# Kernel tuning notes

Hardware: AMD Instinct MI355X
Metric: run time of the kernel (lower is better)

## Reference

```python
import jax, jax.numpy as jnp
import numpy as np

D_MODEL = 192; D_INNER = 384; N_STATE = 16; D_CONV = 4; DT_RANK = 12; DEPTH = 24
PATCH = 16; STRIDE = 16; IMG = 128; EPS = 1e-5


def _ln(x, w, b):
    m = jnp.mean(x, -1, keepdims=True)
    v = jnp.mean((x - m) ** 2, -1, keepdims=True)
    return (x - m) * jax.lax.rsqrt(v + EPS) * w + b


def _mamba_dir(xz, cw, cb, xpw, dpw, dpb, Alog, Dv):
    # xz: (B, L, 2*d_inner); one direction of the bidirectional Mamba mixer
    xp, z = jnp.split(xz, 2, axis=-1)               # (B,L,di) each
    xc = jnp.transpose(xp, (0, 2, 1))               # (B,di,L)
    xc = jnp.pad(xc, ((0, 0), (0, 0), (D_CONV - 1, 0)))  # causal pad
    xc = jax.lax.conv_general_dilated(
        xc, cw, (1,), 'VALID',
        dimension_numbers=('NCH', 'OIH', 'NCH'),
        feature_group_count=D_INNER) + cb[None, :, None]
    u = jax.nn.silu(jnp.transpose(xc, (0, 2, 1)))   # (B,L,di)
    dbl = u @ xpw.T                                  # (B,L,dt_rank+2N)
    dt, Bm, Cm = jnp.split(dbl, [DT_RANK, DT_RANK + N_STATE], axis=-1)
    dt = jax.nn.softplus(dt @ dpw.T + dpb)           # (B,L,di)
    A = -jnp.exp(Alog)                               # (di,N)
    dA = jnp.exp(dt[..., None] * A)                  # (B,L,di,N)
    dBu = (dt * u)[..., None] * Bm[:, :, None, :]    # (B,L,di,N)

    def comb(c1, c2):
        a1, b1 = c1
        a2, b2 = c2
        return a1 * a2, a2 * b1 + b2

    _, h = jax.lax.associative_scan(comb, (dA, dBu), axis=1)
    y = jnp.einsum('bldn,bln->bld', h, Cm) + u * Dv
    return y * jax.nn.silu(z)


def _forward(x, patch_w, patch_b, ln_w, ln_b, in_w,
             cf_w, cf_b, xpf_w, dtf_w, dtf_b, Alog_f, D_f,
             cbk_w, cbk_b, xpb_w, dtb_w, dtb_b, Alog_b, D_b,
             out_w, nf_w, nf_b, head_w, head_b):
    B = x.shape[0]
    p = jax.lax.conv_general_dilated(
        x, patch_w, (STRIDE,) * 3, 'VALID',
        dimension_numbers=('NCDHW', 'OIDHW', 'NCDHW')) + patch_b[None, :, None, None, None]
    hidden = p.reshape(B, D_MODEL, -1).transpose(0, 2, 1)  # (B, L=512, D)
    residual = jnp.zeros_like(hidden)

    xs = (ln_w, ln_b, in_w, cf_w, cf_b, xpf_w, dtf_w, dtf_b, Alog_f, D_f,
          cbk_w, cbk_b, xpb_w, dtb_w, dtb_b, Alog_b, D_b, out_w)

    def step(carry, pl):
        hidden, residual = carry
        (lw, lb, iw, cfw, cfb, xpf, dwf, dbf, Af, Dfv,
         cbw, cbb, xpb, dwb, dbb, Ab, Dbv, ow) = pl
        residual = residual + hidden
        hn = _ln(residual, lw, lb)
        xz = hn @ iw.T                               # (B,L,2di)
        yf = _mamba_dir(xz, cfw, cfb, xpf, dwf, dbf, Af, Dfv)
        yb = jnp.flip(_mamba_dir(jnp.flip(xz, 1), cbw, cbb, xpb, dwb, dbb, Ab, Dbv), 1)
        hidden = (yf + yb) @ ow.T
        return (hidden, residual), None

    (hidden, residual), _ = jax.lax.scan(step, (hidden, residual), xs)
    final = _ln(residual + hidden, nf_w, nf_b)
    feat = final[:, -1, :]                           # final_pool_type='none' -> last token
    return feat @ head_w.T + head_b


def setup_inputs() -> dict:
    key = jax.random.key(0)
    ks = jax.random.split(key, 16)
    rn = lambda k, s, sc=0.02: jax.random.normal(k, s, jnp.float32) * sc
    d = {}
    d['x'] = jax.random.normal(ks[0], (1, 1, IMG, IMG, IMG), jnp.float32)
    d['patch_w'] = rn(ks[1], (D_MODEL, 1, PATCH, PATCH, PATCH), 0.05)
    d['patch_b'] = jnp.zeros((D_MODEL,), jnp.float32)
    d['ln_w'] = jnp.ones((DEPTH, D_MODEL), jnp.float32)
    d['ln_b'] = jnp.zeros((DEPTH, D_MODEL), jnp.float32)
    d['in_w'] = rn(ks[2], (DEPTH, 2 * D_INNER, D_MODEL))
    d['cf_w'] = rn(ks[3], (DEPTH, D_INNER, 1, D_CONV), 0.2)
    d['cf_b'] = jnp.zeros((DEPTH, D_INNER), jnp.float32)
    d['xpf_w'] = rn(ks[4], (DEPTH, DT_RANK + 2 * N_STATE, D_INNER))
    d['dtf_w'] = rn(ks[5], (DEPTH, D_INNER, DT_RANK), 0.1)
    d['dtf_b'] = jnp.full((DEPTH, D_INNER), -4.6, jnp.float32)  # softplus -> dt~0.01
    d['Alog_f'] = jnp.log(jnp.broadcast_to(jnp.arange(1, N_STATE + 1, dtype=jnp.float32), (DEPTH, D_INNER, N_STATE)))
    d['D_f'] = jnp.ones((DEPTH, D_INNER), jnp.float32)
    d['cbk_w'] = rn(ks[6], (DEPTH, D_INNER, 1, D_CONV), 0.2)
    d['cbk_b'] = jnp.zeros((DEPTH, D_INNER), jnp.float32)
    d['xpb_w'] = rn(ks[7], (DEPTH, DT_RANK + 2 * N_STATE, D_INNER))
    d['dtb_w'] = rn(ks[8], (DEPTH, D_INNER, DT_RANK), 0.1)
    d['dtb_b'] = jnp.full((DEPTH, D_INNER), -4.6, jnp.float32)
    d['Alog_b'] = jnp.log(jnp.broadcast_to(jnp.arange(1, N_STATE + 1, dtype=jnp.float32), (DEPTH, D_INNER, N_STATE)))
    d['D_b'] = jnp.ones((DEPTH, D_INNER), jnp.float32)
    d['out_w'] = rn(ks[9], (DEPTH, D_MODEL, D_INNER))
    d['nf_w'] = jnp.ones((D_MODEL,), jnp.float32)
    d['nf_b'] = jnp.zeros((D_MODEL,), jnp.float32)
    d['head_w'] = rn(ks[10], (2, D_MODEL))
    d['head_b'] = jnp.zeros((2,), jnp.float32)
    return d


def reference(x, patch_w, patch_b, ln_w, ln_b, in_w,
              cf_w, cf_b, xpf_w, dtf_w, dtf_b, Alog_f, D_f,
              cbk_w, cbk_b, xpb_w, dtb_w, dtb_b, Alog_b, D_b,
              out_w, nf_w, nf_b, head_w, head_b):
    return _forward(x, patch_w, patch_b, ln_w, ln_b, in_w,
                    cf_w, cf_b, xpf_w, dtf_w, dtf_b, Alog_f, D_f,
                    cbk_w, cbk_b, xpb_w, dtb_w, dtb_b, Alog_b, D_b,
                    out_w, nf_w, nf_b, head_w, head_b)
```

## Files before the change

kernel.cpp:

```cpp
#include <hip/hip_runtime.h>
#include <hip/hip_bf16.h>

#define D_MODEL 192
#define D_INNER 384
#define N_STATE 16
#define DT_RANK 12
#define DEPTH 24
#define SEQ 512
#define NCHUNK 8
#define CLEN 64
#define TS 68
#define AS 33
#define PART_STRIDE (SEQ * D_MODEL)
#define USTR (SEQ * D_INNER)
#define KSPLIT 16

typedef __hip_bfloat16 bf16;
typedef unsigned short u16;

__device__ __forceinline__ float silu_f(float x) { return x / (1.f + __expf(-x)); }
__device__ __forceinline__ float softplus_f(float x) {
    return (x > 20.f) ? x : log1pf(__expf(x));
}
__device__ __forceinline__ float bf2f(unsigned u) {
    return __uint_as_float(u << 16);
}
__device__ __forceinline__ u16 f2bu(float f) {
    bf16 b = __float2bfloat16(f);
    return *reinterpret_cast<u16*>(&b);
}

template<typename T> __device__ __forceinline__ float ld(const void* p, long i) {
    return ((const float*)p)[i];
}
template<> __device__ __forceinline__ float ld<bf16>(const void* p, long i) {
    return bf2f(((const u16*)p)[i]);
}
template<typename T> __device__ __forceinline__ float4 ld4(const void* p, long i) {
    return *(const float4*)((const float*)p + i);
}
template<> __device__ __forceinline__ float4 ld4<bf16>(const void* p, long i) {
    const ushort4 v = *(const ushort4*)((const u16*)p + i);
    return make_float4(bf2f(v.x), bf2f(v.y), bf2f(v.z), bf2f(v.w));
}
template<typename T> __device__ __forceinline__ void st(void* p, int i, float v) {
    ((float*)p)[i] = v;
}
template<> __device__ __forceinline__ void st<bf16>(void* p, int i, float v) {
    ((bf16*)p)[i] = __float2bfloat16(v);
}
__device__ __forceinline__ float dot4(const float4& a, const float4& b) {
    return a.x * b.x + a.y * b.y + a.z * b.z + a.w * b.w;
}
__device__ __forceinline__ void ld8b(const u16* p, float4& a, float4& b) {
    const uint4 u = *(const uint4*)p;
    a.x = bf2f(u.x & 0xffffu); a.y = bf2f(u.x >> 16);
    a.z = bf2f(u.y & 0xffffu); a.w = bf2f(u.y >> 16);
    b.x = bf2f(u.z & 0xffffu); b.y = bf2f(u.z >> 16);
    b.z = bf2f(u.w & 0xffffu); b.w = bf2f(u.w >> 16);
}
__device__ __forceinline__ float4 ld4b(const u16* p) {
    const uint2 u = *(const uint2*)p;
    return make_float4(bf2f(u.x & 0xffffu), bf2f(u.x >> 16),
                       bf2f(u.y & 0xffffu), bf2f(u.y >> 16));
}

struct Prep {
    const void *inw, *ow, *xpwf, *xpwb, *dtwf, *dtwb, *cwf, *cwb,
               *lnw, *lnb, *cbf, *cbb, *dtbf, *dtbb, *Af, *Ab, *Df, *Db,
               *x, *pw, *pb;
    u16 *inwB, *owB, *xpwfB, *xpwbB, *dtwfB, *dtwbB, *cwfB, *cwbB, *xB, *pwB;
    float *lnwF, *lnbF, *cbfF, *cbbF, *dtbfF, *dtbbF, *negAfF, *negAbF, *DfF, *DbF, *pbF;
    int* flag;
};
__device__ void cvtB(const void* s, u16* d, long n, long g, long str, int isb) {
    if (isb) {
        const u16* p = (const u16*)s;
        for (long i = g * 4; i < n; i += str * 4) *(ushort4*)(d + i) = *(const ushort4*)(p + i);
    } else {
        const float* p = (const float*)s;
        for (long i = g * 4; i < n; i += str * 4) {
            const float4 v = *(const float4*)(p + i);
            ushort4 o; o.x = f2bu(v.x); o.y = f2bu(v.y); o.z = f2bu(v.z); o.w = f2bu(v.w);
            *(ushort4*)(d + i) = o;
        }
    }
}
__device__ void cvtF(const void* s, float* d, long n, long g, long str, int isb) {
    if (isb) {
        const u16* p = (const u16*)s;
        for (long i = g * 4; i < n; i += str * 4) {
            const ushort4 v = *(const ushort4*)(p + i);
            *(float4*)(d + i) = make_float4(bf2f(v.x), bf2f(v.y), bf2f(v.z), bf2f(v.w));
        }
    } else {
        const float* p = (const float*)s;
        for (long i = g * 4; i < n; i += str * 4) *(float4*)(d + i) = *(const float4*)(p + i);
    }
}
__device__ void cvtNA(const void* s, float* d, long n, long g, long str, int isb) {
    if (isb) {
        const u16* p = (const u16*)s;
        for (long i = g * 4; i < n; i += str * 4) {
            const ushort4 v = *(const ushort4*)(p + i);
            *(float4*)(d + i) = make_float4(-__expf(bf2f(v.x)), -__expf(bf2f(v.y)),
                                            -__expf(bf2f(v.z)), -__expf(bf2f(v.w)));
        }
    } else {
        const float* p = (const float*)s;
        for (long i = g * 4; i < n; i += str * 4) {
            const float4 v = *(const float4*)(p + i);
            *(float4*)(d + i) = make_float4(-__expf(v.x), -__expf(v.y), -__expf(v.z), -__expf(v.w));
        }
    }
}
__global__ void __launch_bounds__(256) prep_kernel(Prep a) {
    const long g = (long)blockIdx.x * 256 + threadIdx.x;
    const long str = (long)gridDim.x * 256;
    const int isb = (((const unsigned*)a.lnw)[0] != 0x3F800000u);
    if (g == 0) *a.flag = isb;
    cvtB(a.inw,  a.inwB,  3538944, g, str, isb);
    cvtB(a.ow,   a.owB,   1769472, g, str, isb);
    cvtB(a.x,    a.xB,    2097152, g, str, isb);
    cvtB(a.pw,   a.pwB,    786432, g, str, isb);
    cvtB(a.xpwf, a.xpwfB,  405504, g, str, isb);
    cvtB(a.xpwb, a.xpwbB,  405504, g, str, isb);
    cvtB(a.dtwf, a.dtwfB,  110592, g, str, isb);
    cvtB(a.dtwb, a.dtwbB,  110592, g, str, isb);
    cvtB(a.cwf,  a.cwfB,    36864, g, str, isb);
    cvtB(a.cwb,  a.cwbB,    36864, g, str, isb);
    cvtF(a.lnw,  a.lnwF,     4608, g, str, isb);
    cvtF(a.lnb,  a.lnbF,     4608, g, str, isb);
    cvtF(a.cbf,  a.cbfF,     9216, g, str, isb);
    cvtF(a.cbb,  a.cbbF,     9216, g, str, isb);
    cvtF(a.dtbf, a.dtbfF,    9216, g, str, isb);
    cvtF(a.dtbb, a.dtbbF,    9216, g, str, isb);
    cvtF(a.pb,   a.pbF,       192, g, str, isb);
    cvtNA(a.Af,  a.negAfF,  147456, g, str, isb);
    cvtNA(a.Ab,  a.negAbF,  147456, g, str, isb);
    cvtF(a.Df,   a.DfF,      9216, g, str, isb);
    cvtF(a.Db,   a.DbF,      9216, g, str, isb);
}

__global__ void __launch_bounds__(256) patch_kernel(const u16* xB, const u16* pwB,
                                                    const float* pbF, float* hidC) {
    __shared__ float As_[32 * AS];
    __shared__ float Ws[32 * TS];
    const int mt = blockIdx.x, nt = blockIdx.y, ks = blockIdx.z;
    const int m0 = mt * 32, n0 = nt * 64, kk0 = ks * 256;
    const int tid = threadIdx.x, ty = tid >> 4, tx = tid & 15;
    float acc[2][4] = {};
    for (int kk = kk0; kk < kk0 + 256; kk += 32) {
        for (int e = tid; e < 1024; e += 256) {
            const int m = e >> 5, k = e & 31;
            const int kid = kk + k, t = m0 + m;
            const int dz = kid >> 8, dy = (kid >> 4) & 15, dx = kid & 15;
            const int pz = t >> 6, py = (t >> 3) & 7, px = t & 7;
            As_[k * AS + m] = bf2f(xB[(long)(pz * 16 + dz) * 16384 + (py * 16 + dy) * 128 + (px * 16 + dx)]);
        }
        for (int e = tid; e < 2048; e += 256) {
            const int n = e >> 5, k = e & 31;
            Ws[k * TS + n] = bf2f(pwB[(long)(n0 + n) * 4096 + kk + k]);
        }
        __syncthreads();
        #pragma unroll 8
        for (int k = 0; k < 32; ++k) {
            const float a0 = As_[k * AS + ty * 2];
            const float a1 = As_[k * AS + ty * 2 + 1];
            const float4 w4 = *(const float4*)&Ws[k * TS + tx * 4];
            acc[0][0] += a0 * w4.x; acc[0][1] += a0 * w4.y;
            acc[0][2] += a0 * w4.z; acc[0][3] += a0 * w4.w;
            acc[1][0] += a1 * w4.x; acc[1][1] += a1 * w4.y;
            acc[1][2] += a1 * w4.z; acc[1][3] += a1 * w4.w;
        }
        __syncthreads();
    }
    float* C = hidC + (long)ks * PART_STRIDE;
    #pragma unroll
    for (int i = 0; i < 2; ++i) {
        float4 o4 = make_float4(acc[i][0], acc[i][1], acc[i][2], acc[i][3]);
        if (ks == 0) {
            o4.x += pbF[n0 + tx * 4 + 0];
            o4.y += pbF[n0 + tx * 4 + 1];
            o4.z += pbF[n0 + tx * 4 + 2];
            o4.w += pbF[n0 + tx * 4 + 3];
        }
        *(float4*)&C[(m0 + ty * 2 + i) * D_MODEL + n0 + tx * 4] = o4;
    }
}

__global__ void __launch_bounds__(256) fusedA_kernel(int l, int first,
        const float* hidC, const float* y, const float* resIn, float* resOut,
        const float* lnwF, const float* lnbF, const u16* inwB, const u16* owB, float* xz) {
    __shared__ float sy[2 * D_INNER];
    __shared__ float lnS[2 * D_MODEL];
    __shared__ float hnS[2 * D_MODEL];
    const int tid = threadIdx.x;
    const int t0 = blockIdx.x * 2;
    if (!first) {
        for (int i = tid; i < 2 * D_INNER; i += 256) {
            const int tt = i / D_INNER, d = i - tt * D_INNER;
            const long o = (long)(t0 + tt) * D_INNER + d;
            sy[i] = y[o] + y[(long)USTR + o];
        }
    }
    __syncthreads();
    if (tid < D_MODEL) {
        float accB[2];
        if (first) {
            #pragma unroll
            for (int tt = 0; tt < 2; ++tt) {
                float s = 0.f;
                #pragma unroll
                for (int sp = 0; sp < KSPLIT; ++sp)
                    s += hidC[(long)sp * PART_STRIDE + (t0 + tt) * D_MODEL + tid];
                accB[tt] = s;
            }
        } else {
            accB[0] = accB[1] = 0.f;
            const u16* wr = owB + (long)(l - 1) * D_MODEL * D_INNER + (long)tid * D_INNER;
            for (int k = 0; k < D_INNER; k += 8) {
                float4 a, b;
                ld8b(wr + k, a, b);
                accB[0] += dot4(a, *(const float4*)&sy[k]) + dot4(b, *(const float4*)&sy[k + 4]);
                accB[1] += dot4(a, *(const float4*)&sy[D_INNER + k]) + dot4(b, *(const float4*)&sy[D_INNER + k + 4]);
            }
        }
        #pragma unroll
        for (int tt = 0; tt < 2; ++tt) {
            const float rv = accB[tt] + (first ? 0.f : resIn[(t0 + tt) * D_MODEL + tid]);
            lnS[tt * D_MODEL + tid] = rv;
            resOut[(t0 + tt) * D_MODEL + tid] = rv;
        }
    }
    __syncthreads();
    {
        const int w = tid >> 6, lane = tid & 63;
        if (w < 2) {
            const float v0 = lnS[w * D_MODEL + lane];
            const float v1 = lnS[w * D_MODEL + lane + 64];
            const float v2 = lnS[w * D_MODEL + lane + 128];
            float s = v0 + v1 + v2;
            #pragma unroll
            for (int o = 32; o > 0; o >>= 1) s += __shfl_xor(s, o, 64);
            const float mean = s * (1.f / D_MODEL);
            const float d0 = v0 - mean, d1 = v1 - mean, d2 = v2 - mean;
            float s2 = d0 * d0 + d1 * d1 + d2 * d2;
            #pragma unroll
            for (int o = 32; o > 0; o >>= 1) s2 += __shfl_xor(s2, o, 64);
            const float rstd = rsqrtf(s2 * (1.f / D_MODEL) + 1e-5f);
            hnS[w * D_MODEL + lane]       = d0 * rstd * lnwF[l * D_MODEL + lane]       + lnbF[l * D_MODEL + lane];
            hnS[w * D_MODEL + lane + 64]  = d1 * rstd * lnwF[l * D_MODEL + lane + 64]  + lnbF[l * D_MODEL + lane + 64];
            hnS[w * D_MODEL + lane + 128] = d2 * rstd * lnwF[l * D_MODEL + lane + 128] + lnbF[l * D_MODEL + lane + 128];
        }
    }
    __syncthreads();
    float accD[3][2] = {};
    const u16* w0 = inwB + (long)l * 2 * D_INNER * D_MODEL;
    for (int k = 0; k < D_MODEL; k += 8) {
        #pragma unroll
        for (int r = 0; r < 3; ++r) {
            float4 a, b;
            ld8b(w0 + (long)(tid + r * 256) * D_MODEL + k, a, b);
            #pragma unroll
            for (int tt = 0; tt < 2; ++tt) {
                accD[r][tt] += dot4(a, *(const float4*)&hnS[tt * D_MODEL + k])
                             + dot4(b, *(const float4*)&hnS[tt * D_MODEL + k + 4]);
            }
        }
    }
    #pragma unroll
    for (int r = 0; r < 3; ++r)
        #pragma unroll
        for (int tt = 0; tt < 2; ++tt)
            xz[(long)(t0 + tt) * 2 * D_INNER + tid + r * 256] = accD[r][tt];
}

__global__ void __launch_bounds__(256) stage_kernel(int l, const float* xz,
        const u16* cwfB, const float* cbfF, const u16* xpwfB, const u16* dtwfB, const float* dtbfF,
        const u16* cwbB, const float* cbbF, const u16* xpwbB, const u16* dtwbB, const float* dtbbF,
        float* u, float* dbl, float* dt) {
    __shared__ float su[2 * D_INNER];
    __shared__ float dblP[192];
    __shared__ float dblS[96];
    const int dir = blockIdx.y;
    const u16* cwB  = dir ? cwbB  : cwfB;
    const float* cbF = dir ? cbbF : cbfF;
    const u16* xpwB = dir ? xpwbB : xpwfB;
    const u16* dtwB = dir ? dtwbB : dtwfB;
    const float* dtbF = dir ? dtbbF : dtbfF;
    const int tid = threadIdx.x;
    const int t0 = blockIdx.x * 2;
    float* ub = u + (long)dir * USTR;
    for (int i = tid; i < 2 * D_INNER; i += 256) {
        const int tt = i / D_INNER, d = i - tt * D_INNER;
        const int t = t0 + tt;
        const float4 w4 = ld4b(cwB + (long)(l * D_INNER + d) * 4);
        const float cwk[4] = {w4.x, w4.y, w4.z, w4.w};
        float acc = cbF[l * D_INNER + d];
        #pragma unroll
        for (int k = 0; k < 4; ++k) {
            const int ii = t + k - 3;
            if (ii >= 0) {
                const int src = dir ? (511 - ii) : ii;
                acc += xz[(long)src * 2 * D_INNER + d] * cwk[k];
            }
        }
        const float uv = silu_f(acc);
        su[tt * D_INNER + d] = uv;
        ub[(long)t * D_INNER + d] = uv;
    }
    __syncthreads();
    if (tid < 176) {
        const int half = tid / 88;
        const int r = tid - half * 88;
        const int tt = r / 44, out = r - tt * 44;
        const u16* wr = xpwB + (long)(l * 44 + out) * D_INNER;
        const int k0 = half * 192;
        float acc = 0.f;
        for (int k = k0; k < k0 + 192; k += 8) {
            float4 a, b;
            ld8b(wr + k, a, b);
            acc += dot4(a, *(const float4*)&su[tt * D_INNER + k])
                 + dot4(b, *(const float4*)&su[tt * D_INNER + k + 4]);
        }
        dblP[half * 96 + tt * 48 + out] = acc;
    }
    __syncthreads();
    if (tid < 88) {
        const int tt = tid / 44, out = tid - tt * 44;
        const float s = dblP[tt * 48 + out] + dblP[96 + tt * 48 + out];
        dblS[tt * 48 + out] = s;
        dbl[(long)dir * SEQ * 44 + (long)(t0 + tt) * 44 + out] = s;
    }
    __syncthreads();
    float* dtp = dt + (long)dir * USTR;
    for (int i = tid; i < 2 * D_INNER; i += 256) {
        const int tt = i / D_INNER, d = i - tt * D_INNER;
        const u16* wr = dtwB + (long)(l * D_INNER + d) * DT_RANK;
        const float4 wa = ld4b(wr), wb2 = ld4b(wr + 4), wc = ld4b(wr + 8);
        const float* ds = &dblS[tt * 48];
        float acc = dtbF[l * D_INNER + d]
            + wa.x * ds[0] + wa.y * ds[1] + wa.z * ds[2] + wa.w * ds[3]
            + wb2.x * ds[4] + wb2.y * ds[5] + wb2.z * ds[6] + wb2.w * ds[7]
            + wc.x * ds[8] + wc.y * ds[9] + wc.z * ds[10] + wc.w * ds[11];
        dtp[(long)(t0 + tt) * D_INNER + d] = softplus_f(acc);
    }
}

__global__ void __launch_bounds__(256) scan1_kernel(int l, const float* u, const float* dbl,
        const float* dt, const float* negAf, const float* negAb, float* chunkH, float* chunkP) {
    __shared__ float sU[CLEN * 16];
    __shared__ float sDT[CLEN * 16];
    __shared__ float sB[CLEN * 16];
    const int dg = blockIdx.x, chunk = blockIdx.y, dir = blockIdx.z;
    const int tid = threadIdx.x;
    const int ch = tid >> 4, np = tid & 15;
    const int d0 = dg * 16, d = d0 + ch;
    const int t0 = chunk * CLEN;
    const float* ub = u + (long)dir * USTR;
    const float* dtp = dt + (long)dir * USTR;
    const float* db = dbl + (long)dir * SEQ * 44;
    {
        const int t = tid >> 2, dl4 = (tid & 3) * 4;
        const long base = (long)(t0 + t) * D_INNER + d0 + dl4;
        *(float4*)&sU[t * 16 + dl4]  = *(const float4*)&ub[base];
        *(float4*)&sDT[t * 16 + dl4] = *(const float4*)&dtp[base];
        *(float4*)&sB[t * 16 + dl4]  = *(const float4*)&db[(long)(t0 + t) * 44 + DT_RANK + dl4];
    }
    const float* negA = dir ? negAb : negAf;
    const float A = negA[(long)(l * D_INNER + d) * N_STATE + np];
    __syncthreads();
    float h = 0.f, dts = 0.f;
    for (int t = 0; t < CLEN; ++t) {
        const float dtv = sDT[t * 16 + ch];
        h = __expf(dtv * A) * h + (dtv * sU[t * 16 + ch]) * sB[t * 16 + np];
        dts += dtv;
    }
    const long base = ((long)(dir * NCHUNK + chunk) * D_INNER + d) * N_STATE + np;
    chunkH[base] = h;
    chunkP[base] = __expf(A * dts);
}

__global__ void __launch_bounds__(256) scan2_kernel(int l, const float* xz,
        const float* u, const float* dbl, const float* dt,
        const float* negAf, const float* negAb, const float* DfF, const float* DbF,
        const float* chunkH, const float* chunkP, float* y) {
    __shared__ float sU[CLEN * 16];
    __shared__ float sDT[CLEN * 16];
    __shared__ float sBC[CLEN * 32];
    __shared__ float sZ[CLEN * 16];
    __shared__ float sY[CLEN * 16];
    const int dg = blockIdx.x, chunk = blockIdx.y, dir = blockIdx.z;
    const int tid = threadIdx.x;
    const int ch = tid >> 4, np = tid & 15;
    const int d0 = dg * 16, d = d0 + ch;
    const int t0 = chunk * CLEN;
    const float* ub = u + (long)dir * USTR;
    const float* dtp = dt + (long)dir * USTR;
    const float* db = dbl + (long)dir * SEQ * 44;
    float* yb = y + (long)dir * USTR;
    {
        const int t = tid >> 2, dl4 = (tid & 3) * 4;
        const int tg = t0 + t;
        const long base = (long)tg * D_INNER + d0 + dl4;
        *(float4*)&sU[t * 16 + dl4]  = *(const float4*)&ub[base];
        *(float4*)&sDT[t * 16 + dl4] = *(const float4*)&dtp[base];
        const int out_l = dir ? (511 - tg) : tg;
        *(float4*)&sZ[t * 16 + dl4] = *(const float4*)&xz[(long)out_l * 2 * D_INNER + D_INNER + d0 + dl4];
    }
    for (int i = tid; i < 512; i += 256) {
        const int t = i >> 3, j4 = (i & 7) * 4;
        *(float4*)&sBC[t * 32 + j4] = *(const float4*)&db[(long)(t0 + t) * 44 + DT_RANK + j4];
    }
    const float* negA = dir ? negAb : negAf;
    const float* Dp = dir ? DbF : DfF;
    const float A = negA[(long)(l * D_INNER + d) * N_STATE + np];
    const float Dval = Dp[l * D_INNER + d];
    float h = 0.f;
    for (int c = 0; c < chunk; ++c) {
        const long base = ((long)(dir * NCHUNK + c) * D_INNER + d) * N_STATE + np;
        h = chunkP[base] * h + chunkH[base];
    }
    __syncthreads();
    for (int t = 0; t < CLEN; ++t) {
        const float dtv = sDT[t * 16 + ch];
        const float uv = sU[t * 16 + ch];
        h = __expf(dtv * A) * h + (dtv * uv) * sBC[t * 32 + np];
        float part = h * sBC[t * 32 + 16 + np];
        part += __shfl_xor(part, 1, 64);
        part += __shfl_xor(part, 2, 64);
        part += __shfl_xor(part, 4, 64);
        part += __shfl_xor(part, 8, 64);
        if (np == 0)
            sY[t * 16 + ch] = (part + uv * Dval) * silu_f(sZ[t * 16 + ch]);
    }
    __syncthreads();
    {
        const int t = tid >> 2, dl4 = (tid & 3) * 4;
        const int tg = t0 + t;
        const int out_l = dir ? (511 - tg) : tg;
        *(float4*)&yb[(long)out_l * D_INNER + d0 + dl4] = *(const float4*)&sY[t * 16 + dl4];
    }
}

template<typename T>
__device__ void final_body(const float* res, const float* y, const void* ow,
                           const void* nw, const void* nb, const void* hw, const void* hb,
                           void* out, float* syf, float* f, float* red) {
    const int tid = threadIdx.x;
    for (int i = tid; i < D_INNER; i += 192)
        syf[i] = y[(long)511 * D_INNER + i] + y[(long)USTR + 511 * D_INNER + i];
    __syncthreads();
    float acc = 0.f;
    const long wrow = (long)(DEPTH - 1) * D_MODEL * D_INNER + (long)tid * D_INNER;
    for (int k = 0; k < D_INNER; k += 4)
        acc += dot4(ld4<T>(ow, wrow + k), *(const float4*)&syf[k]);
    const float v = res[511 * D_MODEL + tid] + acc;
    float s = v;
    #pragma unroll
    for (int o = 32; o > 0; o >>= 1) s += __shfl_down(s, o, 64);
    if ((tid & 63) == 0) red[tid >> 6] = s;
    __syncthreads();
    const float mean = (red[0] + red[1] + red[2]) * (1.f / D_MODEL);
    const float d = v - mean;
    float s2 = d * d;
    #pragma unroll
    for (int o = 32; o > 0; o >>= 1) s2 += __shfl_down(s2, o, 64);
    if ((tid & 63) == 0) red[3 + (tid >> 6)] = s2;
    __syncthreads();
    const float var = (red[3] + red[4] + red[5]) * (1.f / D_MODEL);
    f[tid] = d * rsqrtf(var + 1e-5f) * ld<T>(nw, tid) + ld<T>(nb, tid);
    __syncthreads();
    if (tid < 2) {
        float a2 = ld<T>(hb, tid);
        for (int c = 0; c < D_MODEL; ++c) a2 += f[c] * ld<T>(hw, tid * D_MODEL + c);
        st<T>(out, tid, a2);
    }
}
__global__ void final_kernel(const int* flag, const float* res, const float* y, const void* ow,
                             const void* nw, const void* nb, const void* hw, const void* hb,
                             void* out) {
    __shared__ float syf[D_INNER];
    __shared__ float f[D_MODEL];
    __shared__ float red[6];
    if (*flag) final_body<bf16>(res, y, ow, nw, nb, hw, hb, out, syf, f, red);
    else       final_body<float>(res, y, ow, nw, nb, hw, hb, out, syf, f, red);
}

extern "C" void kernel_launch(void* const* d_in, const int* in_sizes, int n_in,
                              void* d_out, int out_size, void* d_ws, size_t ws_size,
                              hipStream_t stream) {
    const void* x    = d_in[0];
    const void* pw   = d_in[1];
    const void* pb   = d_in[2];
    const void* lnw  = d_in[3];
    const void* lnb  = d_in[4];
    const void* inw  = d_in[5];
    const void* cfw  = d_in[6];
    const void* cfb  = d_in[7];
    const void* xpfw = d_in[8];
    const void* dtfw = d_in[9];
    const void* dtfb = d_in[10];
    const void* Af   = d_in[11];
    const void* Dfv  = d_in[12];
    const void* cbw  = d_in[13];
    const void* cbb  = d_in[14];
    const void* xpbw = d_in[15];
    const void* dtbw = d_in[16];
    const void* dtbb = d_in[17];
    const void* Ab   = d_in[18];
    const void* Dbv  = d_in[19];
    const void* ow   = d_in[20];
    const void* nfw  = d_in[21];
    const void* nfb  = d_in[22];
    const void* hw   = d_in[23];
    const void* hb   = d_in[24];

    int* flag = (int*)d_ws;
    float* w = (float*)((char*)d_ws + 16);
    float* hidC   = w;  w += KSPLIT * PART_STRIDE;
    float* res0   = w;  w += PART_STRIDE;
    float* res1   = w;  w += PART_STRIDE;
    float* xz     = w;  w += SEQ * 2 * D_INNER;
    float* u      = w;  w += 2 * USTR;
    float* dbl    = w;  w += 2 * SEQ * 44;
    float* dt     = w;  w += 2 * USTR;
    float* y      = w;  w += 2 * USTR;
    float* chunkH = w;  w += 2 * NCHUNK * D_INNER * N_STATE;
    float* chunkP = w;  w += 2 * NCHUNK * D_INNER * N_STATE;
    float* lnwF = w;  w += 4608;
    float* lnbF = w;  w += 4608;
    float* cbfF = w;  w += 9216;
    float* cbbF = w;  w += 9216;
    float* dtbfF = w; w += 9216;
    float* dtbbF = w; w += 9216;
    float* negAfF = w; w += 147456;
    float* negAbF = w; w += 147456;
    float* DfF = w;   w += 9216;
    float* DbF = w;   w += 9216;
    float* pbF = w;   w += 192;
    u16* b = (u16*)w;
    u16* inwB  = b;  b += 3538944;
    u16* owB   = b;  b += 1769472;
    u16* xB    = b;  b += 2097152;
    u16* pwB   = b;  b += 786432;
    u16* xpwfB = b;  b += 405504;
    u16* xpwbB = b;  b += 405504;
    u16* dtwfB = b;  b += 110592;
    u16* dtwbB = b;  b += 110592;
    u16* cwfB  = b;  b += 36864;
    u16* cwbB  = b;  b += 36864;
    float* res[2] = { res0, res1 };

    Prep pa;
    pa.inw = inw; pa.ow = ow; pa.xpwf = xpfw; pa.xpwb = xpbw;
    pa.dtwf = dtfw; pa.dtwb = dtbw; pa.cwf = cfw; pa.cwb = cbw;
    pa.lnw = lnw; pa.lnb = lnb; pa.cbf = cfb; pa.cbb = cbb;
    pa.dtbf = dtfb; pa.dtbb = dtbb; pa.Af = Af; pa.Ab = Ab; pa.Df = Dfv; pa.Db = Dbv;
    pa.x = x; pa.pw = pw; pa.pb = pb;
    pa.inwB = inwB; pa.owB = owB; pa.xpwfB = xpwfB; pa.xpwbB = xpwbB;
    pa.dtwfB = dtwfB; pa.dtwbB = dtwbB; pa.cwfB = cwfB; pa.cwbB = cwbB;
    pa.xB = xB; pa.pwB = pwB;
    pa.lnwF = lnwF; pa.lnbF = lnbF; pa.cbfF = cbfF; pa.cbbF = cbbF;
    pa.dtbfF = dtbfF; pa.dtbbF = dtbbF; pa.negAfF = negAfF; pa.negAbF = negAbF;
    pa.DfF = DfF; pa.DbF = DbF; pa.pbF = pbF; pa.flag = flag;
    prep_kernel<<<1024, 256, 0, stream>>>(pa);

    patch_kernel<<<dim3(16, 3, KSPLIT), 256, 0, stream>>>(xB, pwB, pbF, hidC);

    for (int l = 0; l < DEPTH; ++l) {
        const int first = (l == 0);
        fusedA_kernel<<<256, 256, 0, stream>>>(l, first, hidC, y,
            res[l & 1], res[(l + 1) & 1], lnwF, lnbF, inwB, owB, xz);
        stage_kernel<<<dim3(256, 2), 256, 0, stream>>>(l, xz,
            cwfB, cbfF, xpwfB, dtwfB, dtbfF,
            cwbB, cbbF, xpwbB, dtwbB, dtbbF, u, dbl, dt);
        scan1_kernel<<<dim3(24, NCHUNK, 2), 256, 0, stream>>>(l, u, dbl, dt,
            negAfF, negAbF, chunkH, chunkP);
        scan2_kernel<<<dim3(24, NCHUNK, 2), 256, 0, stream>>>(l, xz, u, dbl, dt,
            negAfF, negAbF, DfF, DbF, chunkH, chunkP, y);
    }

    final_kernel<<<1, 192, 0, stream>>>(flag, res0, y, ow, nfw, nfb, hw, hb, d_out);
}
```

Baseline: 1.896 ms.

## Fuse all per-layer kernels into one persistent kernel with grid barriers

Replaces the prep, patch, per-layer fusedA/stage/scan1/scan2 and final launches with a single persistent mega kernel of 512 blocks that synchronises phases through a software grid barrier built on atomics. The goal is to remove roughly a hundred kernel launches and their inter-kernel gaps, and to keep scan state (A, shared tiles) resident between scan phases. The trade-off is that every block must be co-resident for the barrier to be correct. The spin loop has a timeout that could silently break synchronisation, and idle blocks sit waiting during phases that use only 384 blocks.

```diff
diff --git a/kernel.cpp b/kernel.cpp
--- a/kernel.cpp
+++ b/kernel.cpp
@@ -14,6 +14,7 @@
 #define PART_STRIDE (SEQ * D_MODEL)
 #define USTR (SEQ * D_INNER)
 #define KSPLIT 16
+#define NBLK 512
 
 typedef __hip_bfloat16 bf16;
 typedef unsigned short u16;
@@ -65,14 +66,27 @@
                        bf2f(u.y & 0xffffu), bf2f(u.y >> 16));
 }
 
-struct Prep {
-    const void *inw, *ow, *xpwf, *xpwb, *dtwf, *dtwb, *cwf, *cwb,
-               *lnw, *lnb, *cbf, *cbb, *dtbf, *dtbb, *Af, *Ab, *Df, *Db,
-               *x, *pw, *pb;
-    u16 *inwB, *owB, *xpwfB, *xpwbB, *dtwfB, *dtwbB, *cwfB, *cwbB, *xB, *pwB;
-    float *lnwF, *lnbF, *cbfF, *cbbF, *dtbfF, *dtbbF, *negAfF, *negAbF, *DfF, *DbF, *pbF;
-    int* flag;
-};
+__device__ __forceinline__ void gbar(unsigned* cnt, unsigned* gen) {
+    __syncthreads();
+    if (threadIdx.x == 0) {
+        __threadfence();
+        const unsigned g = __hip_atomic_load(gen, __ATOMIC_RELAXED, __HIP_MEMORY_SCOPE_AGENT);
+        const unsigned prev = __hip_atomic_fetch_add(cnt, 1u, __ATOMIC_ACQ_REL, __HIP_MEMORY_SCOPE_AGENT);
+        if (prev == NBLK - 1u) {
+            __hip_atomic_store(cnt, 0u, __ATOMIC_RELAXED, __HIP_MEMORY_SCOPE_AGENT);
+            __hip_atomic_fetch_add(gen, 1u, __ATOMIC_RELEASE, __HIP_MEMORY_SCOPE_AGENT);
+        } else {
+            int spins = 0;
+            while (__hip_atomic_load(gen, __ATOMIC_RELAXED, __HIP_MEMORY_SCOPE_AGENT) == g) {
+                if (++spins > (1 << 16)) break;
+                __builtin_amdgcn_s_sleep(1);
+            }
+        }
+        __threadfence();
+    }
+    __syncthreads();
+}
+
 __device__ void cvtB(const void* s, u16* d, long n, long g, long str, int isb) {
     if (isb) {
         const u16* p = (const u16*)s;
@@ -114,363 +128,37 @@
         }
     }
 }
-__global__ void __launch_bounds__(256) prep_kernel(Prep a) {
-    const long g = (long)blockIdx.x * 256 + threadIdx.x;
-    const long str = (long)gridDim.x * 256;
-    const int isb = (((const unsigned*)a.lnw)[0] != 0x3F800000u);
-    if (g == 0) *a.flag = isb;
-    cvtB(a.inw,  a.inwB,  3538944, g, str, isb);
-    cvtB(a.ow,   a.owB,   1769472, g, str, isb);
-    cvtB(a.x,    a.xB,    2097152, g, str, isb);
-    cvtB(a.pw,   a.pwB,    786432, g, str, isb);
-    cvtB(a.xpwf, a.xpwfB,  405504, g, str, isb);
-    cvtB(a.xpwb, a.xpwbB,  405504, g, str, isb);
-    cvtB(a.dtwf, a.dtwfB,  110592, g, str, isb);
-    cvtB(a.dtwb, a.dtwbB,  110592, g, str, isb);
-    cvtB(a.cwf,  a.cwfB,    36864, g, str, isb);
-    cvtB(a.cwb,  a.cwbB,    36864, g, str, isb);
-    cvtF(a.lnw,  a.lnwF,     4608, g, str, isb);
-    cvtF(a.lnb,  a.lnbF,     4608, g, str, isb);
-    cvtF(a.cbf,  a.cbfF,     9216, g, str, isb);
-    cvtF(a.cbb,  a.cbbF,     9216, g, str, isb);
-    cvtF(a.dtbf, a.dtbfF,    9216, g, str, isb);
-    cvtF(a.dtbb, a.dtbbF,    9216, g, str, isb);
-    cvtF(a.pb,   a.pbF,       192, g, str, isb);
-    cvtNA(a.Af,  a.negAfF,  147456, g, str, isb);
-    cvtNA(a.Ab,  a.negAbF,  147456, g, str, isb);
-    cvtF(a.Df,   a.DfF,      9216, g, str, isb);
-    cvtF(a.Db,   a.DbF,      9216, g, str, isb);
-}
-
-__global__ void __launch_bounds__(256) patch_kernel(const u16* xB, const u16* pwB,
-                                                    const float* pbF, float* hidC) {
-    __shared__ float As_[32 * AS];
-    __shared__ float Ws[32 * TS];
-    const int mt = blockIdx.x, nt = blockIdx.y, ks = blockIdx.z;
-    const int m0 = mt * 32, n0 = nt * 64, kk0 = ks * 256;
-    const int tid = threadIdx.x, ty = tid >> 4, tx = tid & 15;
-    float acc[2][4] = {};
-    for (int kk = kk0; kk < kk0 + 256; kk += 32) {
-        for (int e = tid; e < 1024; e += 256) {
-            const int m = e >> 5, k = e & 31;
-            const int kid = kk + k, t = m0 + m;
-            const int dz = kid >> 8, dy = (kid >> 4) & 15, dx = kid & 15;
-            const int pz = t >> 6, py = (t >> 3) & 7, px = t & 7;
-            As_[k * AS + m] = bf2f(xB[(long)(pz * 16 + dz) * 16384 + (py * 16 + dy) * 128 + (px * 16 + dx)]);
-        }
-        for (int e = tid; e < 2048; e += 256) {
-            const int n = e >> 5, k = e & 31;
-            Ws[k * TS + n] = bf2f(pwB[(long)(n0 + n) * 4096 + kk + k]);
-        }
-        __syncthreads();
-        #pragma unroll 8
-        for (int k = 0; k < 32; ++k) {
-            const float a0 = As_[k * AS + ty * 2];
-            const float a1 = As_[k * AS + ty * 2 + 1];
-            const float4 w4 = *(const float4*)&Ws[k * TS + tx * 4];
-            acc[0][0] += a0 * w4.x; acc[0][1] += a0 * w4.y;
-            acc[0][2] += a0 * w4.z; acc[0][3] += a0 * w4.w;
-            acc[1][0] += a1 * w4.x; acc[1][1] += a1 * w4.y;
-            acc[1][2] += a1 * w4.z; acc[1][3] += a1 * w4.w;
-        }
-        __syncthreads();
-    }
-    float* C = hidC + (long)ks * PART_STRIDE;
-    #pragma unroll
-    for (int i = 0; i < 2; ++i) {
-        float4 o4 = make_float4(acc[i][0], acc[i][1], acc[i][2], acc[i][3]);
-        if (ks == 0) {
-            o4.x += pbF[n0 + tx * 4 + 0];
-            o4.y += pbF[n0 + tx * 4 + 1];
-            o4.z += pbF[n0 + tx * 4 + 2];
-            o4.w += pbF[n0 + tx * 4 + 3];
-        }
-        *(float4*)&C[(m0 + ty * 2 + i) * D_MODEL + n0 + tx * 4] = o4;
-    }
-}
-
-__global__ void __launch_bounds__(256) fusedA_kernel(int l, int first,
-        const float* hidC, const float* y, const float* resIn, float* resOut,
-        const float* lnwF, const float* lnbF, const u16* inwB, const u16* owB, float* xz) {
-    __shared__ float sy[2 * D_INNER];
-    __shared__ float lnS[2 * D_MODEL];
-    __shared__ float hnS[2 * D_MODEL];
-    const int tid = threadIdx.x;
-    const int t0 = blockIdx.x * 2;
-    if (!first) {
-        for (int i = tid; i < 2 * D_INNER; i += 256) {
-            const int tt = i / D_INNER, d = i - tt * D_INNER;
-            const long o = (long)(t0 + tt) * D_INNER + d;
-            sy[i] = y[o] + y[(long)USTR + o];
-        }
-    }
-    __syncthreads();
-    if (tid < D_MODEL) {
-        float accB[2];
-        if (first) {
-            #pragma unroll
-            for (int tt = 0; tt < 2; ++tt) {
-                float s = 0.f;
-                #pragma unroll
-                for (int sp = 0; sp < KSPLIT; ++sp)
-                    s += hidC[(long)sp * PART_STRIDE + (t0 + tt) * D_MODEL + tid];
-                accB[tt] = s;
-            }
-        } else {
-            accB[0] = accB[1] = 0.f;
-            const u16* wr = owB + (long)(l - 1) * D_MODEL * D_INNER + (long)tid * D_INNER;
-            for (int k = 0; k < D_INNER; k += 8) {
-                float4 a, b;
-                ld8b(wr + k, a, b);
-                accB[0] += dot4(a, *(const float4*)&sy[k]) + dot4(b, *(const float4*)&sy[k + 4]);
-                accB[1] += dot4(a, *(const float4*)&sy[D_INNER + k]) + dot4(b, *(const float4*)&sy[D_INNER + k + 4]);
-            }
-        }
-        #pragma unroll
-        for (int tt = 0; tt < 2; ++tt) {
-            const float rv = accB[tt] + (first ? 0.f : resIn[(t0 + tt) * D_MODEL + tid]);
-            lnS[tt * D_MODEL + tid] = rv;
-            resOut[(t0 + tt) * D_MODEL + tid] = rv;
-        }
-    }
-    __syncthreads();
-    {
-        const int w = tid >> 6, lane = tid & 63;
-        if (w < 2) {
-            const float v0 = lnS[w * D_MODEL + lane];
-            const float v1 = lnS[w * D_MODEL + lane + 64];
-            const float v2 = lnS[w * D_MODEL + lane + 128];
-            float s = v0 + v1 + v2;
-            #pragma unroll
-            for (int o = 32; o > 0; o >>= 1) s += __shfl_xor(s, o, 64);
-            const float mean = s * (1.f / D_MODEL);
-            const float d0 = v0 - mean, d1 = v1 - mean, d2 = v2 - mean;
-            float s2 = d0 * d0 + d1 * d1 + d2 * d2;
-            #pragma unroll
-            for (int o = 32; o > 0; o >>= 1) s2 += __shfl_xor(s2, o, 64);
-            const float rstd = rsqrtf(s2 * (1.f / D_MODEL) + 1e-5f);
-            hnS[w * D_MODEL + lane]       = d0 * rstd * lnwF[l * D_MODEL + lane]       + lnbF[l * D_MODEL + lane];
-            hnS[w * D_MODEL + lane + 64]  = d1 * rstd * lnwF[l * D_MODEL + lane + 64]  + lnbF[l * D_MODEL + lane + 64];
-            hnS[w * D_MODEL + lane + 128] = d2 * rstd * lnwF[l * D_MODEL + lane + 128] + lnbF[l * D_MODEL + lane + 128];
-        }
-    }
-    __syncthreads();
-    float accD[3][2] = {};
-    const u16* w0 = inwB + (long)l * 2 * D_INNER * D_MODEL;
-    for (int k = 0; k < D_MODEL; k += 8) {
-        #pragma unroll
-        for (int r = 0; r < 3; ++r) {
-            float4 a, b;
-            ld8b(w0 + (long)(tid + r * 256) * D_MODEL + k, a, b);
-            #pragma unroll
-            for (int tt = 0; tt < 2; ++tt) {
-                accD[r][tt] += dot4(a, *(const float4*)&hnS[tt * D_MODEL + k])
-                             + dot4(b, *(const float4*)&hnS[tt * D_MODEL + k + 4]);
-            }
-        }
-    }
-    #pragma unroll
-    for (int r = 0; r < 3; ++r)
-        #pragma unroll
-        for (int tt = 0; tt < 2; ++tt)
-            xz[(long)(t0 + tt) * 2 * D_INNER + tid + r * 256] = accD[r][tt];
-}
-
-__global__ void __launch_bounds__(256) stage_kernel(int l, const float* xz,
-        const u16* cwfB, const float* cbfF, const u16* xpwfB, const u16* dtwfB, const float* dtbfF,
-        const u16* cwbB, const float* cbbF, const u16* xpwbB, const u16* dtwbB, const float* dtbbF,
-        float* u, float* dbl, float* dt) {
-    __shared__ float su[2 * D_INNER];
-    __shared__ float dblP[192];
-    __shared__ float dblS[96];
-    const int dir = blockIdx.y;
-    const u16* cwB  = dir ? cwbB  : cwfB;
-    const float* cbF = dir ? cbbF : cbfF;
-    const u16* xpwB = dir ? xpwbB : xpwfB;
-    const u16* dtwB = dir ? dtwbB : dtwfB;
-    const float* dtbF = dir ? dtbbF : dtbfF;
-    const int tid = threadIdx.x;
-    const int t0 = blockIdx.x * 2;
-    float* ub = u + (long)dir * USTR;
-    for (int i = tid; i < 2 * D_INNER; i += 256) {
-        const int tt = i / D_INNER, d = i - tt * D_INNER;
-        const int t = t0 + tt;
-        const float4 w4 = ld4b(cwB + (long)(l * D_INNER + d) * 4);
-        const float cwk[4] = {w4.x, w4.y, w4.z, w4.w};
-        float acc = cbF[l * D_INNER + d];
-        #pragma unroll
-        for (int k = 0; k < 4; ++k) {
-            const int ii = t + k - 3;
-            if (ii >= 0) {
-                const int src = dir ? (511 - ii) : ii;
-                acc += xz[(long)src * 2 * D_INNER + d] * cwk[k];
-            }
-        }
-        const float uv = silu_f(acc);
-        su[tt * D_INNER + d] = uv;
-        ub[(long)t * D_INNER + d] = uv;
-    }
-    __syncthreads();
-    if (tid < 176) {
-        const int half = tid / 88;
-        const int r = tid - half * 88;
-        const int tt = r / 44, out = r - tt * 44;
-        const u16* wr = xpwB + (long)(l * 44 + out) * D_INNER;
-        const int k0 = half * 192;
-        float acc = 0.f;
-        for (int k = k0; k < k0 + 192; k += 8) {
-            float4 a, b;
-            ld8b(wr + k, a, b);
-            acc += dot4(a, *(const float4*)&su[tt * D_INNER + k])
-                 + dot4(b, *(const float4*)&su[tt * D_INNER + k + 4]);
-        }
-        dblP[half * 96 + tt * 48 + out] = acc;
-    }
-    __syncthreads();
-    if (tid < 88) {
-        const int tt = tid / 44, out = tid - tt * 44;
-        const float s = dblP[tt * 48 + out] + dblP[96 + tt * 48 + out];
-        dblS[tt * 48 + out] = s;
-        dbl[(long)dir * SEQ * 44 + (long)(t0 + tt) * 44 + out] = s;
-    }
-    __syncthreads();
-    float* dtp = dt + (long)dir * USTR;
-    for (int i = tid; i < 2 * D_INNER; i += 256) {
-        const int tt = i / D_INNER, d = i - tt * D_INNER;
-        const u16* wr = dtwB + (long)(l * D_INNER + d) * DT_RANK;
-        const float4 wa = ld4b(wr), wb2 = ld4b(wr + 4), wc = ld4b(wr + 8);
-        const float* ds = &dblS[tt * 48];
-        float acc = dtbF[l * D_INNER + d]
-            + wa.x * ds[0] + wa.y * ds[1] + wa.z * ds[2] + wa.w * ds[3]
-            + wb2.x * ds[4] + wb2.y * ds[5] + wb2.z * ds[6] + wb2.w * ds[7]
-            + wc.x * ds[8] + wc.y * ds[9] + wc.z * ds[10] + wc.w * ds[11];
-        dtp[(long)(t0 + tt) * D_INNER + d] = softplus_f(acc);
-    }
-}
-
-__global__ void __launch_bounds__(256) scan1_kernel(int l, const float* u, const float* dbl,
-        const float* dt, const float* negAf, const float* negAb, float* chunkH, float* chunkP) {
-    __shared__ float sU[CLEN * 16];
-    __shared__ float sDT[CLEN * 16];
-    __shared__ float sB[CLEN * 16];
-    const int dg = blockIdx.x, chunk = blockIdx.y, dir = blockIdx.z;
-    const int tid = threadIdx.x;
-    const int ch = tid >> 4, np = tid & 15;
-    const int d0 = dg * 16, d = d0 + ch;
-    const int t0 = chunk * CLEN;
-    const float* ub = u + (long)dir * USTR;
-    const float* dtp = dt + (long)dir * USTR;
-    const float* db = dbl + (long)dir * SEQ * 44;
-    {
-        const int t = tid >> 2, dl4 = (tid & 3) * 4;
-        const long base = (long)(t0 + t) * D_INNER + d0 + dl4;
-        *(float4*)&sU[t * 16 + dl4]  = *(const float4*)&ub[base];
-        *(float4*)&sDT[t * 16 + dl4] = *(const float4*)&dtp[base];
-        *(float4*)&sB[t * 16 + dl4]  = *(const float4*)&db[(long)(t0 + t) * 44 + DT_RANK + dl4];
-    }
-    const float* negA = dir ? negAb : negAf;
-    const float A = negA[(long)(l * D_INNER + d) * N_STATE + np];
-    __syncthreads();
-    float h = 0.f, dts = 0.f;
-    for (int t = 0; t < CLEN; ++t) {
-        const float dtv = sDT[t * 16 + ch];
-        h = __expf(dtv * A) * h + (dtv * sU[t * 16 + ch]) * sB[t * 16 + np];
-        dts += dtv;
-    }
-    const long base = ((long)(dir * NCHUNK + chunk) * D_INNER + d) * N_STATE + np;
-    chunkH[base] = h;
-    chunkP[base] = __expf(A * dts);
-}
-
-__global__ void __launch_bounds__(256) scan2_kernel(int l, const float* xz,
-        const float* u, const float* dbl, const float* dt,
-        const float* negAf, const float* negAb, const float* DfF, const float* DbF,
-        const float* chunkH, const float* chunkP, float* y) {
-    __shared__ float sU[CLEN * 16];
-    __shared__ float sDT[CLEN * 16];
-    __shared__ float sBC[CLEN * 32];
-    __shared__ float sZ[CLEN * 16];
-    __shared__ float sY[CLEN * 16];
-    const int dg = blockIdx.x, chunk = blockIdx.y, dir = blockIdx.z;
-    const int tid = threadIdx.x;
-    const int ch = tid >> 4, np = tid & 15;
-    const int d0 = dg * 16, d = d0 + ch;
-    const int t0 = chunk * CLEN;
-    const float* ub = u + (long)dir * USTR;
-    const float* dtp = dt + (long)dir * USTR;
-    const float* db = dbl + (long)dir * SEQ * 44;
-    float* yb = y + (long)dir * USTR;
-    {
-        const int t = tid >> 2, dl4 = (tid & 3) * 4;
-        const int tg = t0 + t;
-        const long base = (long)tg * D_INNER + d0 + dl4;
-        *(float4*)&sU[t * 16 + dl4]  = *(const float4*)&ub[base];
-        *(float4*)&sDT[t * 16 + dl4] = *(const float4*)&dtp[base];
-        const int out_l = dir ? (511 - tg) : tg;
-        *(float4*)&sZ[t * 16 + dl4] = *(const float4*)&xz[(long)out_l * 2 * D_INNER + D_INNER + d0 + dl4];
-    }
-    for (int i = tid; i < 512; i += 256) {
-        const int t = i >> 3, j4 = (i & 7) * 4;
-        *(float4*)&sBC[t * 32 + j4] = *(const float4*)&db[(long)(t0 + t) * 44 + DT_RANK + j4];
-    }
-    const float* negA = dir ? negAb : negAf;
-    const float* Dp = dir ? DbF : DfF;
-    const float A = negA[(long)(l * D_INNER + d) * N_STATE + np];
-    const float Dval = Dp[l * D_INNER + d];
-    float h = 0.f;
-    for (int c = 0; c < chunk; ++c) {
-        const long base = ((long)(dir * NCHUNK + c) * D_INNER + d) * N_STATE + np;
-        h = chunkP[base] * h + chunkH[base];
-    }
-    __syncthreads();
-    for (int t = 0; t < CLEN; ++t) {
-        const float dtv = sDT[t * 16 + ch];
-        const float uv = sU[t * 16 + ch];
-        h = __expf(dtv * A) * h + (dtv * uv) * sBC[t * 32 + np];
-        float part = h * sBC[t * 32 + 16 + np];
-        part += __shfl_xor(part, 1, 64);
-        part += __shfl_xor(part, 2, 64);
-        part += __shfl_xor(part, 4, 64);
-        part += __shfl_xor(part, 8, 64);
-        if (np == 0)
-            sY[t * 16 + ch] = (part + uv * Dval) * silu_f(sZ[t * 16 + ch]);
-    }
-    __syncthreads();
-    {
-        const int t = tid >> 2, dl4 = (tid & 3) * 4;
-        const int tg = t0 + t;
-        const int out_l = dir ? (511 - tg) : tg;
-        *(float4*)&yb[(long)out_l * D_INNER + d0 + dl4] = *(const float4*)&sY[t * 16 + dl4];
-    }
-}
 
 template<typename T>
-__device__ void final_body(const float* res, const float* y, const void* ow,
-                           const void* nw, const void* nb, const void* hw, const void* hb,
-                           void* out, float* syf, float* f, float* red) {
-    const int tid = threadIdx.x;
-    for (int i = tid; i < D_INNER; i += 192)
+__device__ void final_phase(int tid, const float* res, const float* y, const void* ow,
+                            const void* nw, const void* nb, const void* hw, const void* hb,
+                            void* out, float* syf, float* f, float* red) {
+    for (int i = tid; i < D_INNER; i += 256)
         syf[i] = y[(long)511 * D_INNER + i] + y[(long)USTR + 511 * D_INNER + i];
     __syncthreads();
-    float acc = 0.f;
-    const long wrow = (long)(DEPTH - 1) * D_MODEL * D_INNER + (long)tid * D_INNER;
-    for (int k = 0; k < D_INNER; k += 4)
-        acc += dot4(ld4<T>(ow, wrow + k), *(const float4*)&syf[k]);
-    const float v = res[511 * D_MODEL + tid] + acc;
+    float v = 0.f;
+    if (tid < D_MODEL) {
+        float acc = 0.f;
+        const long wrow = (long)(DEPTH - 1) * D_MODEL * D_INNER + (long)tid * D_INNER;
+        for (int k = 0; k < D_INNER; k += 4)
+            acc += dot4(ld4<T>(ow, wrow + k), *(const float4*)&syf[k]);
+        v = res[511 * D_MODEL + tid] + acc;
+    }
     float s = v;
     #pragma unroll
     for (int o = 32; o > 0; o >>= 1) s += __shfl_down(s, o, 64);
-    if ((tid & 63) == 0) red[tid >> 6] = s;
+    if ((tid & 63) == 0 && tid < D_MODEL) red[tid >> 6] = s;
     __syncthreads();
     const float mean = (red[0] + red[1] + red[2]) * (1.f / D_MODEL);
-    const float d = v - mean;
+    const float d = (tid < D_MODEL) ? (v - mean) : 0.f;
     float s2 = d * d;
     #pragma unroll
     for (int o = 32; o > 0; o >>= 1) s2 += __shfl_down(s2, o, 64);
-    if ((tid & 63) == 0) red[3 + (tid >> 6)] = s2;
+    if ((tid & 63) == 0 && tid < D_MODEL) red[3 + (tid >> 6)] = s2;
     __syncthreads();
     const float var = (red[3] + red[4] + red[5]) * (1.f / D_MODEL);
-    f[tid] = d * rsqrtf(var + 1e-5f) * ld<T>(nw, tid) + ld<T>(nb, tid);
+    if (tid < D_MODEL)
+        f[tid] = d * rsqrtf(var + 1e-5f) * ld<T>(nw, tid) + ld<T>(nb, tid);
     __syncthreads();
     if (tid < 2) {
         float a2 = ld<T>(hb, tid);
@@ -478,19 +166,352 @@
         st<T>(out, tid, a2);
     }
 }
-__global__ void final_kernel(const int* flag, const float* res, const float* y, const void* ow,
-                             const void* nw, const void* nb, const void* hw, const void* hb,
-                             void* out) {
-    __shared__ float syf[D_INNER];
-    __shared__ float f[D_MODEL];
-    __shared__ float red[6];
-    if (*flag) final_body<bf16>(res, y, ow, nw, nb, hw, hb, out, syf, f, red);
-    else       final_body<float>(res, y, ow, nw, nb, hw, hb, out, syf, f, red);
+
+struct MegaArgs {
+    const void *x, *pw, *pb, *lnw, *lnb, *inw, *cfw, *cfb, *xpfw, *dtfw, *dtfb, *Af, *Dfv;
+    const void *cbw, *cbb, *xpbw, *dtbw, *dtbb, *Ab, *Dbv, *ow, *nfw, *nfb, *hw, *hb;
+    void* out;
+    unsigned* bar;
+    float *hidC, *res0, *res1, *xz, *u, *dbl, *dt, *y, *chunkH, *chunkP;
+    float *lnwF, *lnbF, *cbfF, *cbbF, *dtbfF, *dtbbF, *negAfF, *negAbF, *DfF, *DbF, *pbF;
+    u16 *inwB, *owB, *xB, *pwB, *xpwfB, *xpwbB, *dtwfB, *dtwbB, *cwfB, *cwbB;
+};
+
+__global__ void init_kernel(unsigned* bar) { bar[0] = 0; bar[32] = 0; }
+
+__global__ void __launch_bounds__(256, 2) mega_kernel(MegaArgs a) {
+    __shared__ float smem[6144];
+    const int bid = blockIdx.x;
+    const int tid = threadIdx.x;
+    unsigned* bcnt = a.bar;
+    unsigned* bgen = a.bar + 32;
+    const int isb = (((const unsigned*)a.lnw)[0] != 0x3F800000u);
+
+    {
+        const long g = (long)bid * 256 + tid;
+        const long str = (long)NBLK * 256;
+        cvtB(a.inw,  a.inwB,  3538944, g, str, isb);
+        cvtB(a.ow,   a.owB,   1769472, g, str, isb);
+        cvtB(a.x,    a.xB,    2097152, g, str, isb);
+        cvtB(a.pw,   a.pwB,    786432, g, str, isb);
+        cvtB(a.xpfw, a.xpwfB,  405504, g, str, isb);
+        cvtB(a.xpbw, a.xpwbB,  405504, g, str, isb);
+        cvtB(a.dtfw, a.dtwfB,  110592, g, str, isb);
+        cvtB(a.dtbw, a.dtwbB,  110592, g, str, isb);
+        cvtB(a.cfw,  a.cwfB,    36864, g, str, isb);
+        cvtB(a.cbw,  a.cwbB,    36864, g, str, isb);
+        cvtF(a.lnw,  a.lnwF,     4608, g, str, isb);
+        cvtF(a.lnb,  a.lnbF,     4608, g, str, isb);
+        cvtF(a.cfb,  a.cbfF,     9216, g, str, isb);
+        cvtF(a.cbb,  a.cbbF,     9216, g, str, isb);
+        cvtF(a.dtfb, a.dtbfF,    9216, g, str, isb);
+        cvtF(a.dtbb, a.dtbbF,    9216, g, str, isb);
+        cvtF(a.pb,   a.pbF,       192, g, str, isb);
+        cvtNA(a.Af,  a.negAfF,  147456, g, str, isb);
+        cvtNA(a.Ab,  a.negAbF,  147456, g, str, isb);
+        cvtF(a.Dfv,  a.DfF,      9216, g, str, isb);
+        cvtF(a.Dbv,  a.DbF,      9216, g, str, isb);
+    }
+    gbar(bcnt, bgen);
+
+    {
+        float* As_ = smem;
+        float* Ws  = smem + 1056;
+        const int ty = tid >> 4, tx = tid & 15;
+        for (int unit = bid; unit < 768; unit += NBLK) {
+            const int mt = unit & 15, nt = (unit >> 4) % 3, ks = unit / 48;
+            const int m0 = mt * 32, n0 = nt * 64, kk0 = ks * 256;
+            float acc[2][4] = {};
+            for (int kk = kk0; kk < kk0 + 256; kk += 32) {
+                for (int e = tid; e < 1024; e += 256) {
+                    const int m = e >> 5, k = e & 31;
+                    const int kid = kk + k, t = m0 + m;
+                    const int dz = kid >> 8, dy = (kid >> 4) & 15, dx = kid & 15;
+                    const int pz = t >> 6, py = (t >> 3) & 7, px = t & 7;
+                    As_[k * AS + m] = bf2f(a.xB[(long)(pz * 16 + dz) * 16384 + (py * 16 + dy) * 128 + (px * 16 + dx)]);
+                }
+                for (int e = tid; e < 2048; e += 256) {
+                    const int n = e >> 5, k = e & 31;
+                    Ws[k * TS + n] = bf2f(a.pwB[(long)(n0 + n) * 4096 + kk + k]);
+                }
+                __syncthreads();
+                #pragma unroll 8
+                for (int k = 0; k < 32; ++k) {
+                    const float a0 = As_[k * AS + ty * 2];
+                    const float a1 = As_[k * AS + ty * 2 + 1];
+                    const float4 w4 = *(const float4*)&Ws[k * TS + tx * 4];
+                    acc[0][0] += a0 * w4.x; acc[0][1] += a0 * w4.y;
+                    acc[0][2] += a0 * w4.z; acc[0][3] += a0 * w4.w;
+                    acc[1][0] += a1 * w4.x; acc[1][1] += a1 * w4.y;
+                    acc[1][2] += a1 * w4.z; acc[1][3] += a1 * w4.w;
+                }
+                __syncthreads();
+            }
+            float* C = a.hidC + (long)ks * PART_STRIDE;
+            #pragma unroll
+            for (int i = 0; i < 2; ++i) {
+                float4 o4 = make_float4(acc[i][0], acc[i][1], acc[i][2], acc[i][3]);
+                if (ks == 0) {
+                    o4.x += a.pbF[n0 + tx * 4 + 0];
+                    o4.y += a.pbF[n0 + tx * 4 + 1];
+                    o4.z += a.pbF[n0 + tx * 4 + 2];
+                    o4.w += a.pbF[n0 + tx * 4 + 3];
+                }
+                *(float4*)&C[(m0 + ty * 2 + i) * D_MODEL + n0 + tx * 4] = o4;
+            }
+        }
+    }
+    gbar(bcnt, bgen);
+
+    const int ch = tid >> 4, np = tid & 15;
+    float* sU  = smem;
+    float* sDT = smem + 1024;
+    float* sBC = smem + 2048;
+    float* sZ  = smem + 4096;
+    float* sY  = smem + 5120;
+    int dg = 0, chunk = 0, dir2 = 0;
+    float Areg = 0.f, Dval = 0.f;
+
+    for (int l = 0; l < DEPTH; ++l) {
+        const int first = (l == 0);
+        const float* resIn = (l & 1) ? a.res1 : a.res0;
+        float* resOut      = (l & 1) ? a.res0 : a.res1;
+
+        if (bid < 256) {
+            float* sy  = smem;
+            float* lnS = smem + 768;
+            float* hnS = smem + 1152;
+            const int t0 = bid * 2;
+            if (!first) {
+                for (int i = tid; i < 2 * D_INNER; i += 256) {
+                    const int tt = i / D_INNER, d = i - tt * D_INNER;
+                    const long o = (long)(t0 + tt) * D_INNER + d;
+                    sy[i] = a.y[o] + a.y[(long)USTR + o];
+                }
+            }
+            __syncthreads();
+            if (tid < D_MODEL) {
+                float accB[2];
+                if (first) {
+                    #pragma unroll
+                    for (int tt = 0; tt < 2; ++tt) {
+                        float s = 0.f;
+                        #pragma unroll
+                        for (int sp = 0; sp < KSPLIT; ++sp)
+                            s += a.hidC[(long)sp * PART_STRIDE + (t0 + tt) * D_MODEL + tid];
+                        accB[tt] = s;
+                    }
+                } else {
+                    accB[0] = accB[1] = 0.f;
+                    const u16* wr = a.owB + (long)(l - 1) * D_MODEL * D_INNER + (long)tid * D_INNER;
+                    for (int k = 0; k < D_INNER; k += 8) {
+                        float4 va, vb;
+                        ld8b(wr + k, va, vb);
+                        accB[0] += dot4(va, *(const float4*)&sy[k]) + dot4(vb, *(const float4*)&sy[k + 4]);
+                        accB[1] += dot4(va, *(const float4*)&sy[D_INNER + k]) + dot4(vb, *(const float4*)&sy[D_INNER + k + 4]);
+                    }
+                }
+                #pragma unroll
+                for (int tt = 0; tt < 2; ++tt) {
+                    const float rv = accB[tt] + (first ? 0.f : resIn[(t0 + tt) * D_MODEL + tid]);
+                    lnS[tt * D_MODEL + tid] = rv;
+                    resOut[(t0 + tt) * D_MODEL + tid] = rv;
+                }
+            }
+            __syncthreads();
+            {
+                const int w = tid >> 6, lane = tid & 63;
+                if (w < 2) {
+                    const float v0 = lnS[w * D_MODEL + lane];
+                    const float v1 = lnS[w * D_MODEL + lane + 64];
+                    const float v2 = lnS[w * D_MODEL + lane + 128];
+                    float s = v0 + v1 + v2;
+                    #pragma unroll
+                    for (int o = 32; o > 0; o >>= 1) s += __shfl_xor(s, o, 64);
+                    const float mean = s * (1.f / D_MODEL);
+                    const float d0 = v0 - mean, d1 = v1 - mean, d2 = v2 - mean;
+                    float s2 = d0 * d0 + d1 * d1 + d2 * d2;
+                    #pragma unroll
+                    for (int o = 32; o > 0; o >>= 1) s2 += __shfl_xor(s2, o, 64);
+                    const float rstd = rsqrtf(s2 * (1.f / D_MODEL) + 1e-5f);
+                    hnS[w * D_MODEL + lane]       = d0 * rstd * a.lnwF[l * D_MODEL + lane]       + a.lnbF[l * D_MODEL + lane];
+                    hnS[w * D_MODEL + lane + 64]  = d1 * rstd * a.lnwF[l * D_MODEL + lane + 64]  + a.lnbF[l * D_MODEL + lane + 64];
+                    hnS[w * D_MODEL + lane + 128] = d2 * rstd * a.lnwF[l * D_MODEL + lane + 128] + a.lnbF[l * D_MODEL + lane + 128];
+                }
+            }
+            __syncthreads();
+            float accD[3][2] = {};
+            const u16* w0 = a.inwB + (long)l * 2 * D_INNER * D_MODEL;
+            for (int k = 0; k < D_MODEL; k += 8) {
+                #pragma unroll
+                for (int r = 0; r < 3; ++r) {
+                    float4 va, vb;
+                    ld8b(w0 + (long)(tid + r * 256) * D_MODEL + k, va, vb);
+                    #pragma unroll
+                    for (int tt = 0; tt < 2; ++tt) {
+                        accD[r][tt] += dot4(va, *(const float4*)&hnS[tt * D_MODEL + k])
+                                     + dot4(vb, *(const float4*)&hnS[tt * D_MODEL + k + 4]);
+                    }
+                }
+            }
+            #pragma unroll
+            for (int r = 0; r < 3; ++r)
+                #pragma unroll
+                for (int tt = 0; tt < 2; ++tt)
+                    a.xz[(long)(t0 + tt) * 2 * D_INNER + tid + r * 256] = accD[r][tt];
+        }
+        gbar(bcnt, bgen);
+
+        {
+            float* su   = smem;
+            float* dblP = smem + 768;
+            float* dblS = smem + 960;
+            const int dir = bid >> 8;
+            const u16* cwB   = dir ? a.cwbB  : a.cwfB;
+            const float* cbF = dir ? a.cbbF  : a.cbfF;
+            const u16* xpwB  = dir ? a.xpwbB : a.xpwfB;
+            const u16* dtwB  = dir ? a.dtwbB : a.dtwfB;
+            const float* dtbF = dir ? a.dtbbF : a.dtbfF;
+            const int t0 = (bid & 255) * 2;
+            float* ub = a.u + (long)dir * USTR;
+            for (int i = tid; i < 2 * D_INNER; i += 256) {
+                const int tt = i / D_INNER, d = i - tt * D_INNER;
+                const int t = t0 + tt;
+                const float4 w4 = ld4b(cwB + (long)(l * D_INNER + d) * 4);
+                const float cwk[4] = {w4.x, w4.y, w4.z, w4.w};
+                float acc = cbF[l * D_INNER + d];
+                #pragma unroll
+                for (int k = 0; k < 4; ++k) {
+                    const int ii = t + k - 3;
+                    if (ii >= 0) {
+                        const int src = dir ? (511 - ii) : ii;
+                        acc += a.xz[(long)src * 2 * D_INNER + d] * cwk[k];
+                    }
+                }
+                const float uv = silu_f(acc);
+                su[tt * D_INNER + d] = uv;
+                ub[(long)t * D_INNER + d] = uv;
+            }
+            __syncthreads();
+            if (tid < 176) {
+                const int half = tid / 88;
+                const int r = tid - half * 88;
+                const int tt = r / 44, out = r - tt * 44;
+                const u16* wr = xpwB + (long)(l * 44 + out) * D_INNER;
+                const int k0 = half * 192;
+                float acc = 0.f;
+                for (int k = k0; k < k0 + 192; k += 8) {
+                    float4 va, vb;
+                    ld8b(wr + k, va, vb);
+                    acc += dot4(va, *(const float4*)&su[tt * D_INNER + k])
+                         + dot4(vb, *(const float4*)&su[tt * D_INNER + k + 4]);
+                }
+                dblP[half * 96 + tt * 48 + out] = acc;
+            }
+            __syncthreads();
+            if (tid < 88) {
+                const int tt = tid / 44, out = tid - tt * 44;
+                const float s = dblP[tt * 48 + out] + dblP[96 + tt * 48 + out];
+                dblS[tt * 48 + out] = s;
+                a.dbl[(long)dir * SEQ * 44 + (long)(t0 + tt) * 44 + out] = s;
+            }
+            __syncthreads();
+            float* dtp = a.dt + (long)dir * USTR;
+            for (int i = tid; i < 2 * D_INNER; i += 256) {
+                const int tt = i / D_INNER, d = i - tt * D_INNER;
+                const u16* wr = dtwB + (long)(l * D_INNER + d) * DT_RANK;
+                const float4 wa = ld4b(wr), wb2 = ld4b(wr + 4), wc = ld4b(wr + 8);
+                const float* ds = &dblS[tt * 48];
+                float acc = dtbF[l * D_INNER + d]
+                    + wa.x * ds[0] + wa.y * ds[1] + wa.z * ds[2] + wa.w * ds[3]
+                    + wb2.x * ds[4] + wb2.y * ds[5] + wb2.z * ds[6] + wb2.w * ds[7]
+                    + wc.x * ds[8] + wc.y * ds[9] + wc.z * ds[10] + wc.w * ds[11];
+                dtp[(long)(t0 + tt) * D_INNER + d] = softplus_f(acc);
+            }
+        }
+        gbar(bcnt, bgen);
+
+        if (bid < 384) {
+            dg = bid % 24; chunk = (bid / 24) & 7; dir2 = bid / 192;
+            const int d0 = dg * 16, d = d0 + ch;
+            const int t0s = chunk * CLEN;
+            const float* ub  = a.u  + (long)dir2 * USTR;
+            const float* dtp = a.dt + (long)dir2 * USTR;
+            const float* db  = a.dbl + (long)dir2 * SEQ * 44;
+            {
+                const int t = tid >> 2, dl4 = (tid & 3) * 4;
+                const int tg = t0s + t;
+                const long base = (long)tg * D_INNER + d0 + dl4;
+                *(float4*)&sU[t * 16 + dl4]  = *(const float4*)&ub[base];
+                *(float4*)&sDT[t * 16 + dl4] = *(const float4*)&dtp[base];
+                const int out_l = dir2 ? (511 - tg) : tg;
+                *(float4*)&sZ[t * 16 + dl4] = *(const float4*)&a.xz[(long)out_l * 2 * D_INNER + D_INNER + d0 + dl4];
+            }
+            for (int i = tid; i < 512; i += 256) {
+                const int t = i >> 3, j4 = (i & 7) * 4;
+                *(float4*)&sBC[t * 32 + j4] = *(const float4*)&db[(long)(t0s + t) * 44 + DT_RANK + j4];
+            }
+            const float* negA = dir2 ? a.negAbF : a.negAfF;
+            Areg = negA[(long)(l * D_INNER + d) * N_STATE + np];
+            Dval = (dir2 ? a.DbF : a.DfF)[l * D_INNER + d];
+            __syncthreads();
+            float h = 0.f, dts = 0.f;
+            for (int t = 0; t < CLEN; ++t) {
+                const float dtv = sDT[t * 16 + ch];
+                h = __expf(dtv * Areg) * h + (dtv * sU[t * 16 + ch]) * sBC[t * 32 + np];
+                dts += dtv;
+            }
+            const long cb = ((long)(dir2 * NCHUNK + chunk) * D_INNER + d) * N_STATE + np;
+            a.chunkH[cb] = h;
+            a.chunkP[cb] = __expf(Areg * dts);
+        }
+        gbar(bcnt, bgen);
+
+        if (bid < 384) {
+            const int d0 = dg * 16, d = d0 + ch;
+            const int t0s = chunk * CLEN;
+            float h = 0.f;
+            for (int c = 0; c < chunk; ++c) {
+                const long cb = ((long)(dir2 * NCHUNK + c) * D_INNER + d) * N_STATE + np;
+                h = a.chunkP[cb] * h + a.chunkH[cb];
+            }
+            for (int t = 0; t < CLEN; ++t) {
+                const float dtv = sDT[t * 16 + ch];
+                const float uv = sU[t * 16 + ch];
+                h = __expf(dtv * Areg) * h + (dtv * uv) * sBC[t * 32 + np];
+                float part = h * sBC[t * 32 + 16 + np];
+                part += __shfl_xor(part, 1, 64);
+                part += __shfl_xor(part, 2, 64);
+                part += __shfl_xor(part, 4, 64);
+                part += __shfl_xor(part, 8, 64);
+                if (np == 0)
+                    sY[t * 16 + ch] = (part + uv * Dval) * silu_f(sZ[t * 16 + ch]);
+            }
+            __syncthreads();
+            {
+                const int t = tid >> 2, dl4 = (tid & 3) * 4;
+                const int tg = t0s + t;
+                const int out_l = dir2 ? (511 - tg) : tg;
+                float* yb = a.y + (long)dir2 * USTR;
+                *(float4*)&yb[(long)out_l * D_INNER + d0 + dl4] = *(const float4*)&sY[t * 16 + dl4];
+            }
+        }
+        gbar(bcnt, bgen);
+    }
+
+    if (bid == 0) {
+        float* syf = smem;
+        float* f   = smem + 384;
+        float* red = smem + 576;
+        if (isb) final_phase<bf16>(tid, a.res0, a.y, a.ow, a.nfw, a.nfb, a.hw, a.hb, a.out, syf, f, red);
+        else     final_phase<float>(tid, a.res0, a.y, a.ow, a.nfw, a.nfb, a.hw, a.hb, a.out, syf, f, red);
+    }
 }
 
 extern "C" void kernel_launch(void* const* d_in, const int* in_sizes, int n_in,
                               void* d_out, int out_size, void* d_ws, size_t ws_size,
                               hipStream_t stream) {
+    (void)in_sizes; (void)n_in; (void)out_size; (void)ws_size;
     const void* x    = d_in[0];
     const void* pw   = d_in[1];
     const void* pb   = d_in[2];
@@ -517,8 +538,8 @@
     const void* hw   = d_in[23];
     const void* hb   = d_in[24];
 
-    int* flag = (int*)d_ws;
-    float* w = (float*)((char*)d_ws + 16);
+    unsigned* bar = (unsigned*)d_ws;
+    float* w = (float*)((char*)d_ws + 256);
     float* hidC   = w;  w += KSPLIT * PART_STRIDE;
     float* res0   = w;  w += PART_STRIDE;
     float* res1   = w;  w += PART_STRIDE;
@@ -551,36 +572,23 @@
     u16* dtwbB = b;  b += 110592;
     u16* cwfB  = b;  b += 36864;
     u16* cwbB  = b;  b += 36864;
-    float* res[2] = { res0, res1 };
-
-    Prep pa;
-    pa.inw = inw; pa.ow = ow; pa.xpwf = xpfw; pa.xpwb = xpbw;
-    pa.dtwf = dtfw; pa.dtwb = dtbw; pa.cwf = cfw; pa.cwb = cbw;
-    pa.lnw = lnw; pa.lnb = lnb; pa.cbf = cfb; pa.cbb = cbb;
-    pa.dtbf = dtfb; pa.dtbb = dtbb; pa.Af = Af; pa.Ab = Ab; pa.Df = Dfv; pa.Db = Dbv;
-    pa.x = x; pa.pw = pw; pa.pb = pb;
-    pa.inwB = inwB; pa.owB = owB; pa.xpwfB = xpwfB; pa.xpwbB = xpwbB;
-    pa.dtwfB = dtwfB; pa.dtwbB = dtwbB; pa.cwfB = cwfB; pa.cwbB = cwbB;
-    pa.xB = xB; pa.pwB = pwB;
-    pa.lnwF = lnwF; pa.lnbF = lnbF; pa.cbfF = cbfF; pa.cbbF = cbbF;
-    pa.dtbfF = dtbfF; pa.dtbbF = dtbbF; pa.negAfF = negAfF; pa.negAbF = negAbF;
-    pa.DfF = DfF; pa.DbF = DbF; pa.pbF = pbF; pa.flag = flag;
-    prep_kernel<<<1024, 256, 0, stream>>>(pa);
-
-    patch_kernel<<<dim3(16, 3, KSPLIT), 256, 0, stream>>>(xB, pwB, pbF, hidC);
-
-    for (int l = 0; l < DEPTH; ++l) {
-        const int first = (l == 0);
-        fusedA_kernel<<<256, 256, 0, stream>>>(l, first, hidC, y,
-            res[l & 1], res[(l + 1) & 1], lnwF, lnbF, inwB, owB, xz);
-        stage_kernel<<<dim3(256, 2), 256, 0, stream>>>(l, xz,
-            cwfB, cbfF, xpwfB, dtwfB, dtbfF,
-            cwbB, cbbF, xpwbB, dtwbB, dtbbF, u, dbl, dt);
-        scan1_kernel<<<dim3(24, NCHUNK, 2), 256, 0, stream>>>(l, u, dbl, dt,
-            negAfF, negAbF, chunkH, chunkP);
-        scan2_kernel<<<dim3(24, NCHUNK, 2), 256, 0, stream>>>(l, xz, u, dbl, dt,
-            negAfF, negAbF, DfF, DbF, chunkH, chunkP, y);
-    }
-
-    final_kernel<<<1, 192, 0, stream>>>(flag, res0, y, ow, nfw, nfb, hw, hb, d_out);
-}
+
+    MegaArgs ma;
+    ma.x = x; ma.pw = pw; ma.pb = pb; ma.lnw = lnw; ma.lnb = lnb; ma.inw = inw;
+    ma.cfw = cfw; ma.cfb = cfb; ma.xpfw = xpfw; ma.dtfw = dtfw; ma.dtfb = dtfb;
+    ma.Af = Af; ma.Dfv = Dfv; ma.cbw = cbw; ma.cbb = cbb; ma.xpbw = xpbw;
+    ma.dtbw = dtbw; ma.dtbb = dtbb; ma.Ab = Ab; ma.Dbv = Dbv; ma.ow = ow;
+    ma.nfw = nfw; ma.nfb = nfb; ma.hw = hw; ma.hb = hb; ma.out = d_out;
+    ma.bar = bar;
+    ma.hidC = hidC; ma.res0 = res0; ma.res1 = res1; ma.xz = xz; ma.u = u;
+    ma.dbl = dbl; ma.dt = dt; ma.y = y; ma.chunkH = chunkH; ma.chunkP = chunkP;
+    ma.lnwF = lnwF; ma.lnbF = lnbF; ma.cbfF = cbfF; ma.cbbF = cbbF;
+    ma.dtbfF = dtbfF; ma.dtbbF = dtbbF; ma.negAfF = negAfF; ma.negAbF = negAbF;
+    ma.DfF = DfF; ma.DbF = DbF; ma.pbF = pbF;
+    ma.inwB = inwB; ma.owB = owB; ma.xB = xB; ma.pwB = pwB;
+    ma.xpwfB = xpwfB; ma.xpwbB = xpwbB; ma.dtwfB = dtwfB; ma.dtwbB = dtwbB;
+    ma.cwfB = cwfB; ma.cwbB = cwbB;
+
+    init_kernel<<<1, 1, 0, stream>>>(bar);
+    mega_kernel<<<NBLK, 256, 0, stream>>>(ma);
+}
```

After: 4.617 ms. 2.43x slower.
